# Kernel tuning notes

Hardware: AMD Instinct MI355X
Metric: run time of the kernel (lower is better)

Reference implementation:

```python
import jax, jax.numpy as jnp
import numpy as np


def setup_inputs() -> dict:
    key = jax.random.key(0)
    k1, k2 = jax.random.split(key)
    B, C, H, W = 16, 512, 64, 64
    x = jax.random.normal(k1, (B, C, H, W), dtype=jnp.float32)
    gamma = jax.random.normal(k2, (1,), dtype=jnp.float32)
    return {"x": x, "gamma": gamma}


def reference(x, gamma):
    # x: [B, C, H, W]
    B, C, H, W = x.shape
    q = x.reshape(B, C, H * W)              # query = key = value = flattened x
    # energy[b, i, j] = <channel_i, channel_j>  -> [B, C, C]
    energy = jnp.einsum('bin,bjn->bij', q, q)
    # attention = softmax(max(energy, -1) - energy) over last dim
    logits = jnp.max(energy, axis=-1, keepdims=True) - energy
    attention = jax.nn.softmax(logits, axis=-1)
    out = jnp.einsum('bij,bjn->bin', attention, q).reshape(B, C, H, W)
    return gamma * out + x
```

## Files before the change

kernel.cpp:

```cpp
#include <hip/hip_runtime.h>
#include <hip/hip_bf16.h>
#include <cstdint>


typedef short    bf16x8 __attribute__((ext_vector_type(8)));
typedef float    f32x4  __attribute__((ext_vector_type(4)));
typedef uint16_t u16x4  __attribute__((ext_vector_type(4)));
typedef uint16_t u16x8  __attribute__((ext_vector_type(8)));

#define AS1 __attribute__((address_space(1)))
#define AS3 __attribute__((address_space(3)))

__device__ __forceinline__ void load_lds16(const void* g, void* l) {
  __builtin_amdgcn_global_load_lds((const AS1 unsigned int*)g,
                                   (AS3 unsigned int*)l, 16, 0, 0);
}

static constexpr int  BB  = 16, C = 512, N = 4096;
static constexpr long XSZ = (long)BB * C * N;
static constexpr long ESZ = (long)BB * C * C;
static constexpr int  ZSPLIT = 8;

__global__ __launch_bounds__(256) void cam_splitT(
    const float* __restrict__ x, uint16_t* __restrict__ qT) {
  __shared__ uint16_t tile[64][68];
  const int t  = threadIdx.x;
  const int b  = blockIdx.z;
  const int c0 = blockIdx.y * 64;
  const int n0 = blockIdx.x * 64;
  const float* xb  = x  + (long)b * C * N;
  uint16_t*    qTb = qT + (long)b * N * C;
  const int cl = t >> 4;
  const int nl = (t & 15) * 4;
  for (int r = 0; r < 4; ++r) {
    const int  c   = cl + r * 16;
    const long off = (long)(c0 + c) * N + n0 + nl;
    const float4 v = *(const float4*)(xb + off);
    const float vv[4] = {v.x, v.y, v.z, v.w};
    u16x4 hv;
    for (int k = 0; k < 4; ++k) {
      __hip_bfloat16 hb = __float2bfloat16(vv[k]);
      hv[k] = *(uint16_t*)&hb;
    }
    *(u16x4*)&tile[c][nl] = hv;
  }
  __syncthreads();
  for (int r = 0; r < 4; ++r) {
    const int n  = cl + r * 16;
    const int cc = (t & 15) * 4;
    u16x4 o = {tile[cc + 0][n], tile[cc + 1][n], tile[cc + 2][n], tile[cc + 3][n]};
    *(u16x4*)(qTb + (long)(n0 + n) * C + c0 + cc) = o;
  }
}

__device__ __forceinline__ void split4(float4 v, uint2& h, uint2& l) {
  const uint32_t u0 = __float_as_uint(v.x), u1 = __float_as_uint(v.y);
  const uint32_t u2 = __float_as_uint(v.z), u3 = __float_as_uint(v.w);
  const float r0 = v.x - __uint_as_float(u0 & 0xffff0000u);
  const float r1 = v.y - __uint_as_float(u1 & 0xffff0000u);
  const float r2 = v.z - __uint_as_float(u2 & 0xffff0000u);
  const float r3 = v.w - __uint_as_float(u3 & 0xffff0000u);
  h.x = (u0 >> 16) | (u1 & 0xffff0000u);
  h.y = (u2 >> 16) | (u3 & 0xffff0000u);
  l.x = (__float_as_uint(r0) >> 16) | (__float_as_uint(r1) & 0xffff0000u);
  l.y = (__float_as_uint(r2) >> 16) | (__float_as_uint(r3) & 0xffff0000u);
}

__global__ __launch_bounds__(256) void cam_energy(
    const float* __restrict__ x, float* __restrict__ E) {
  __shared__ uint16_t smem[4 * 128 * 32];
  const int tid = threadIdx.x;
  const int wave = tid >> 6, lane = tid & 63;
  const int idx = blockIdx.x;
  const int low = idx & 7, chunk = idx >> 3;
  const int gh = chunk / 10, t = chunk - gh * 10;
  const int g  = gh * 8 + low;
  const int b  = g >> 3, z = g & 7;
  const int ti = (t < 4) ? 0 : (t < 7) ? 1 : (t < 9) ? 2 : 3;
  const int tj = t - ((ti * (9 - ti)) >> 1) + ti;
  const bool diag = (ti == tj);
  const int i0 = ti * 128, j0 = tj * 128;
  const float* xb = x + (long)b * C * N;
  const int sr = tid >> 3;
  const int sc = (tid & 7) * 4;
  const float* pA = xb + (long)(i0 + sr) * N + sc;
  const float* pB = xb + (long)(j0 + sr) * N + sc;
  uint16_t* smAh = smem;
  uint16_t* smAl = smem + 4096;
  uint16_t* smBh = diag ? smem        : smem + 8192;
  uint16_t* smBl = diag ? smem + 4096 : smem + 12288;
  const int wr = wave >> 1, wc = wave & 1;
  const int m16 = lane & 15, q4 = lane >> 4;
  f32x4 acc[4][4] = {};
  const int k0 = z * (N / ZSPLIT), kend = k0 + N / ZSPLIT;
  float4 ra[4], rb[4];
  #pragma unroll
  for (int p = 0; p < 4; ++p) {
    ra[p] = *(const float4*)(pA + k0 + (long)p * 32 * N);
    if (!diag) rb[p] = *(const float4*)(pB + k0 + (long)p * 32 * N);
  }
  for (int kk = k0; kk < kend; kk += 32) {
    #pragma unroll
    for (int p = 0; p < 4; ++p) {
      const int row = p * 32 + sr;
      uint2 h, l;
      split4(ra[p], h, l);
      *(uint2*)(smAh + row * 32 + sc) = h;
      *(uint2*)(smAl + row * 32 + sc) = l;
      if (!diag) {
        split4(rb[p], h, l);
        *(uint2*)(smem + 8192 + row * 32 + sc) = h;
        *(uint2*)(smem + 12288 + row * 32 + sc) = l;
      }
    }
    __syncthreads();
    const int kn = (kk + 32 < kend) ? kk + 32 : k0;
    #pragma unroll
    for (int p = 0; p < 4; ++p) {
      ra[p] = *(const float4*)(pA + kn + (long)p * 32 * N);
      if (!diag) rb[p] = *(const float4*)(pB + kn + (long)p * 32 * N);
    }
    bf16x8 ah[4], al[4], bh[4], bl[4];
    for (int i = 0; i < 4; ++i) {
      const int r = wr * 64 + i * 16 + m16;
      ah[i] = *(const bf16x8*)(smAh + r * 32 + q4 * 8);
      al[i] = *(const bf16x8*)(smAl + r * 32 + q4 * 8);
    }
    for (int j = 0; j < 4; ++j) {
      const int r = wc * 64 + j * 16 + m16;
      bh[j] = *(const bf16x8*)(smBh + r * 32 + q4 * 8);
      bl[j] = *(const bf16x8*)(smBl + r * 32 + q4 * 8);
    }
    for (int i = 0; i < 4; ++i)
      for (int j = 0; j < 4; ++j) {
        acc[i][j] = __builtin_amdgcn_mfma_f32_16x16x32_bf16(ah[i], bh[j], acc[i][j], 0, 0, 0);
        acc[i][j] = __builtin_amdgcn_mfma_f32_16x16x32_bf16(ah[i], bl[j], acc[i][j], 0, 0, 0);
        acc[i][j] = __builtin_amdgcn_mfma_f32_16x16x32_bf16(al[i], bh[j], acc[i][j], 0, 0, 0);
      }
    __syncthreads();
  }
  float* Eb = E + (long)z * ESZ + (long)b * C * C;
  for (int i = 0; i < 4; ++i) {
    const int rb_ = i0 + wr * 64 + i * 16 + q4 * 4;
    for (int j = 0; j < 4; ++j) {
      const int cc = j0 + wc * 64 + j * 16 + m16;
      for (int r = 0; r < 4; ++r)
        Eb[(long)(rb_ + r) * C + cc] = acc[i][j][r];
      if (!diag)
        *(f32x4*)(Eb + (long)cc * C + rb_) = acc[i][j];
    }
  }
}

__global__ __launch_bounds__(256) void cam_softmax(
    const float* __restrict__ E, uint16_t* __restrict__ attn) {
  const int t = threadIdx.x;
  const int wave = t >> 6, lane = t & 63;
  const long row = (long)blockIdx.x * 4 + wave;
  const float* e = E + row * C + lane * 8;
  float vv[8] = {};
  for (int z = 0; z < ZSPLIT; ++z) {
    const float4 a0 = *(const float4*)(e + (long)z * ESZ);
    const float4 a1 = *(const float4*)(e + (long)z * ESZ + 4);
    vv[0] += a0.x; vv[1] += a0.y; vv[2] += a0.z; vv[3] += a0.w;
    vv[4] += a1.x; vv[5] += a1.y; vv[6] += a1.z; vv[7] += a1.w;
  }
  float m = vv[0];
  for (int k = 1; k < 8; ++k) m = fminf(m, vv[k]);
  for (int s = 32; s; s >>= 1) m = fminf(m, __shfl_xor(m, s));
  float w[8], sum = 0.f;
  for (int k = 0; k < 8; ++k) { w[k] = __expf(m - vv[k]); sum += w[k]; }
  for (int s = 32; s; s >>= 1) sum += __shfl_xor(sum, s);
  const float inv = 1.0f / sum;
  u16x8 o;
  for (int k = 0; k < 8; ++k) {
    __hip_bfloat16 h = __float2bfloat16(w[k] * inv);
    o[k] = *(uint16_t*)&h;
  }
  *(u16x8*)(attn + row * C + lane * 8) = o;
}

__global__ __launch_bounds__(256) void cam_pv(
    const uint16_t* __restrict__ attn, const uint16_t* __restrict__ qT,
    const float* __restrict__ x, const float* __restrict__ gamma,
    float* __restrict__ out) {
  __shared__ uint16_t smem[2 * 128 * 64];
  const int t = threadIdx.x;
  const int wave = t >> 6, lane = t & 63;
  const int b  = blockIdx.z;
  const int i0 = blockIdx.y * 128;
  const int n0 = blockIdx.x * 128;
  const uint16_t* Ab = attn + (long)b * C * C;
  const uint16_t* Tb = qT   + (long)b * N * C;
  const int lrow8 = lane >> 3;
  const int lk8   = (lane & 7) * 8;
  const int wr = wave >> 1, wc = wave & 1;
  const int m16 = lane & 15, q4 = lane >> 4;
  f32x4 acc[4][4] = {};
  for (int kk = 0; kk < C; kk += 64) {
    for (int s = 0; s < 4; ++s) {
      const int row = (s * 4 + wave) * 8 + lrow8;
      const uint32_t loff = (uint32_t)(s * 4 + wave) * 1024;
      char* lp = (char*)smem + loff;
      load_lds16(Ab + (long)(i0 + row) * C + kk + lk8, lp);
      load_lds16(Tb + (long)(n0 + row) * C + kk + lk8, lp + 16384);
    }
    __syncthreads();
    for (int h = 0; h < 2; ++h) {
      bf16x8 a[4], bb[4];
      for (int i = 0; i < 4; ++i)
        a[i]  = *(const bf16x8*)(smem +        (wr * 64 + i * 16 + m16) * 64 + h * 32 + q4 * 8);
      for (int j = 0; j < 4; ++j)
        bb[j] = *(const bf16x8*)(smem + 8192 + (wc * 64 + j * 16 + m16) * 64 + h * 32 + q4 * 8);
      for (int i = 0; i < 4; ++i)
        for (int j = 0; j < 4; ++j)
          acc[i][j] = __builtin_amdgcn_mfma_f32_16x16x32_bf16(a[i], bb[j], acc[i][j], 0, 0, 0);
    }
    __syncthreads();
  }
  const float g = gamma[0];
  const float* xb = x   + (long)b * C * N;
  float*       ob = out + (long)b * C * N;
  for (int i = 0; i < 4; ++i) {
    const int rb = i0 + wr * 64 + i * 16 + q4 * 4;
    for (int j = 0; j < 4; ++j) {
      const int cc = n0 + wc * 64 + j * 16 + m16;
      for (int r = 0; r < 4; ++r) {
        const long idx = (long)(rb + r) * N + cc;
        ob[idx] = g * acc[i][j][r] + xb[idx];
      }
    }
  }
}

extern "C" void kernel_launch(void* const* d_in, const int* in_sizes, int n_in,
                              void* d_out, int out_size, void* d_ws, size_t ws_size,
                              hipStream_t stream) {
  const float* x     = (const float*)d_in[0];
  const float* gamma = (const float*)d_in[1];
  float* out = (float*)d_out;
  char*  ws  = (char*)d_ws;
  uint16_t* qT   = (uint16_t*)ws;
  float*    E    = (float*)  (ws + XSZ * 2);
  uint16_t* attn = (uint16_t*)(ws + XSZ * 2 + (long)ZSPLIT * ESZ * 4);

  cam_splitT <<<dim3(N / 64, C / 64, BB), 256, 0, stream>>>(x, qT);
  cam_energy <<<dim3(1280),               256, 0, stream>>>(x, E);
  cam_softmax<<<dim3((BB * C) / 4),       256, 0, stream>>>(E, attn);
  cam_pv     <<<dim3(N / 128, C / 128, BB), 256, 0, stream>>>(attn, qT, x, gamma, out);
}
```

Measured before the change: 414.6 us.

## Swizzle LDS tiles and double-buffer the PV kernel's global-to-LDS loads

New measurement: 414.8 us. No clear change (+0.1%).

```diff
diff --git a/kernel.cpp b/kernel.cpp
--- a/kernel.cpp
+++ b/kernel.cpp
@@ -91,6 +91,7 @@
   uint16_t* smBl = diag ? smem + 4096 : smem + 12288;
   const int wr = wave >> 1, wc = wave & 1;
   const int m16 = lane & 15, q4 = lane >> 4;
+  const int usw = (q4 ^ ((m16 >> 1) & 3)) * 8;
   f32x4 acc[4][4] = {};
   const int k0 = z * (N / ZSPLIT), kend = k0 + N / ZSPLIT;
   float4 ra[4], rb[4];
@@ -103,14 +104,15 @@
     #pragma unroll
     for (int p = 0; p < 4; ++p) {
       const int row = p * 32 + sr;
+      const int scs = sc ^ (((row >> 1) & 3) << 3);
       uint2 h, l;
       split4(ra[p], h, l);
-      *(uint2*)(smAh + row * 32 + sc) = h;
-      *(uint2*)(smAl + row * 32 + sc) = l;
+      *(uint2*)(smAh + row * 32 + scs) = h;
+      *(uint2*)(smAl + row * 32 + scs) = l;
       if (!diag) {
         split4(rb[p], h, l);
-        *(uint2*)(smem + 8192 + row * 32 + sc) = h;
-        *(uint2*)(smem + 12288 + row * 32 + sc) = l;
+        *(uint2*)(smem + 8192  + row * 32 + scs) = h;
+        *(uint2*)(smem + 12288 + row * 32 + scs) = l;
       }
     }
     __syncthreads();
@@ -123,13 +125,13 @@
     bf16x8 ah[4], al[4], bh[4], bl[4];
     for (int i = 0; i < 4; ++i) {
       const int r = wr * 64 + i * 16 + m16;
-      ah[i] = *(const bf16x8*)(smAh + r * 32 + q4 * 8);
-      al[i] = *(const bf16x8*)(smAl + r * 32 + q4 * 8);
+      ah[i] = *(const bf16x8*)(smAh + r * 32 + usw);
+      al[i] = *(const bf16x8*)(smAl + r * 32 + usw);
     }
     for (int j = 0; j < 4; ++j) {
       const int r = wc * 64 + j * 16 + m16;
-      bh[j] = *(const bf16x8*)(smBh + r * 32 + q4 * 8);
-      bl[j] = *(const bf16x8*)(smBl + r * 32 + q4 * 8);
+      bh[j] = *(const bf16x8*)(smBh + r * 32 + usw);
+      bl[j] = *(const bf16x8*)(smBl + r * 32 + usw);
     }
     for (int i = 0; i < 4; ++i)
       for (int j = 0; j < 4; ++j) {
@@ -184,7 +186,7 @@
     const uint16_t* __restrict__ attn, const uint16_t* __restrict__ qT,
     const float* __restrict__ x, const float* __restrict__ gamma,
     float* __restrict__ out) {
-  __shared__ uint16_t smem[2 * 128 * 64];
+  __shared__ uint16_t smem[2 * 8192];
   const int t = threadIdx.x;
   const int wave = t >> 6, lane = t & 63;
   const int b  = blockIdx.z;
@@ -192,31 +194,47 @@
   const int n0 = blockIdx.x * 128;
   const uint16_t* Ab = attn + (long)b * C * C;
   const uint16_t* Tb = qT   + (long)b * N * C;
-  const int lrow8 = lane >> 3;
-  const int lk8   = (lane & 7) * 8;
   const int wr = wave >> 1, wc = wave & 1;
   const int m16 = lane & 15, q4 = lane >> 4;
+  const int usw = (q4 ^ ((m16 >> 1) & 3)) * 8;
   f32x4 acc[4][4] = {};
-  for (int kk = 0; kk < C; kk += 64) {
-    for (int s = 0; s < 4; ++s) {
-      const int row = (s * 4 + wave) * 8 + lrow8;
-      const uint32_t loff = (uint32_t)(s * 4 + wave) * 1024;
-      char* lp = (char*)smem + loff;
-      load_lds16(Ab + (long)(i0 + row) * C + kk + lk8, lp);
-      load_lds16(Tb + (long)(n0 + row) * C + kk + lk8, lp + 16384);
-    }
-    __syncthreads();
-    for (int h = 0; h < 2; ++h) {
-      bf16x8 a[4], bb[4];
-      for (int i = 0; i < 4; ++i)
-        a[i]  = *(const bf16x8*)(smem +        (wr * 64 + i * 16 + m16) * 64 + h * 32 + q4 * 8);
+
+  auto stage = [&](int p, int kk) {
+    #pragma unroll
+    for (int s = 0; s < 2; ++s) {
+      const int li  = s * 256 + t;
+      const int row = li >> 2;
+      const int col = ((li & 3) ^ ((row >> 1) & 3)) * 8;
+      uint16_t* lp = smem + p * 8192 + li * 8;
+      load_lds16(Ab + (long)(i0 + row) * C + kk + col, lp);
+      load_lds16(Tb + (long)(n0 + row) * C + kk + col, lp + 4096);
+    }
+  };
+
+  stage(0, 0);
+  asm volatile("s_waitcnt vmcnt(0)" ::: "memory");
+  __builtin_amdgcn_s_barrier();
+  constexpr int NK = C / 32;
+  for (int tk = 0; tk < NK; ++tk) {
+    const int cur = tk & 1;
+    if (tk + 1 < NK) stage(cur ^ 1, (tk + 1) * 32);
+    const uint16_t* sa = smem + cur * 8192;
+    bf16x8 a[4], bv[4];
+    #pragma unroll
+    for (int i = 0; i < 4; ++i)
+      a[i]  = *(const bf16x8*)(sa +        (wr * 64 + i * 16 + m16) * 32 + usw);
+    #pragma unroll
+    for (int j = 0; j < 4; ++j)
+      bv[j] = *(const bf16x8*)(sa + 4096 + (wc * 64 + j * 16 + m16) * 32 + usw);
+    asm volatile("s_waitcnt lgkmcnt(0)" ::: "memory");
+    __builtin_amdgcn_sched_barrier(0);
+    #pragma unroll
+    for (int i = 0; i < 4; ++i)
+      #pragma unroll
       for (int j = 0; j < 4; ++j)
-        bb[j] = *(const bf16x8*)(smem + 8192 + (wc * 64 + j * 16 + m16) * 64 + h * 32 + q4 * 8);
-      for (int i = 0; i < 4; ++i)
-        for (int j = 0; j < 4; ++j)
-          acc[i][j] = __builtin_amdgcn_mfma_f32_16x16x32_bf16(a[i], bb[j], acc[i][j], 0, 0, 0);
-    }
-    __syncthreads();
+        acc[i][j] = __builtin_amdgcn_mfma_f32_16x16x32_bf16(a[i], bv[j], acc[i][j], 0, 0, 0);
+    asm volatile("s_waitcnt vmcnt(0)" ::: "memory");
+    __builtin_amdgcn_s_barrier();
   }
   const float g = gamma[0];
   const float* xb = x   + (long)b * C * N;
```
